# Optimization experiments

Measured on AMD Instinct MI355X. Metric: run time of the kernel, lower is better.

## Reference

```python
import jax, jax.numpy as jnp
import numpy as np

PI = 3.141592653
PC_RANGE = np.array([-140.8, -40.0, -3.0, 140.8, 40.0, 1.0], np.float32)
IOU_THR = 0.1


def limit_period(val, offset=0.5, period=2 * PI):
    return val - jnp.floor(val / period + offset) * period


def pairwise_iou3d(boxes):
    # Axis-aligned 3D IoU approximation of the external boxes_iou3d_gpu CUDA kernel
    # (kernel source not provided). boxes: [N,7] = x,y,z,h,w,l,yaw; extents x<-l, y<-w, z<-h.
    c = boxes[:, :3]
    d = boxes[:, jnp.array([5, 4, 3])]
    lo = c - d * 0.5
    hi = c + d * 0.5
    inter = jnp.clip(jnp.minimum(hi[:, None, :], hi[None, :, :]) - jnp.maximum(lo[:, None, :], lo[None, :, :]), 0.0)
    inter_v = inter.prod(-1)                       # [N,N]
    vol = d.prod(-1)                               # [N]
    return inter_v / jnp.maximum(vol[:, None] + vol[None, :] - inter_v, 1e-8)


def cluster_assign(iou):
    # Greedy sequential clustering: repeatedly take the first unassigned box and
    # assign every box with iou > 0.1 (including already-assigned ones -> overwrite)
    # to a new cluster id. Equivalent to the original while-loop since an index,
    # once nonzero, never returns to zero, so the "first zero" scans left-to-right.
    iou = jax.lax.stop_gradient(iou)
    n = iou.shape[0]

    def body(i, carry):
        idx, cid = carry
        is_new = idx[i] == 0
        idx = jnp.where(is_new & (iou[i] > IOU_THR), cid, idx)
        return idx, cid + jnp.where(is_new, 1, 0).astype(jnp.int32)

    idx0 = jnp.zeros(n, jnp.int32)
    idx, cid = jax.lax.fori_loop(0, n, body, (idx0, jnp.int32(1)))
    return idx, cid


def cluster_fusion(boxes, scores, indices):
    n = boxes.shape[0]
    ids = jnp.arange(1, n + 1, dtype=jnp.int32)
    M = indices[None, :] == ids[:, None]            # [K,N] membership, K==N (padded)
    s_m = jnp.where(M, scores[None, :], 0.0)        # masked scores
    s_sum = s_m.sum(1)
    s_norm = s_m / jnp.maximum(s_sum, 1e-12)[:, None]
    dirs = boxes[:, 6]
    ref_idx = jnp.argmax(jnp.where(M, scores[None, :], -jnp.inf), axis=1)
    ref_dir = dirs[ref_idx]                         # yaw of max-score box per cluster
    diff = jnp.abs(dirs[None, :] - ref_dir[:, None])
    diff = jnp.where(diff > PI, 2 * PI - diff, diff)
    gt = diff > PI / 2
    score_gt = (s_m * gt).sum(1)
    score_le = s_sum - score_gt
    flip = jnp.where((score_gt <= score_le)[:, None], gt, ~gt)
    dirs_adj = limit_period(dirs[None, :] + PI * flip)
    theta = jnp.arctan2((jnp.sin(dirs_adj) * s_norm).sum(1), (jnp.cos(dirs_adj) * s_norm).sum(1))
    center_dim = s_norm @ boxes[:, :6]              # [K,6] score-weighted fusion
    boxes_fused = jnp.concatenate([center_dim, theta[:, None]], axis=1)
    # score fusion: sum_i s_sorted[i] ** (i+1), clipped to 1 (zeros from padding contribute 0)
    s_sorted = jnp.sort(s_m, axis=1)[:, ::-1]
    powers = jnp.arange(1, n + 1, dtype=jnp.float32)
    s_fused = jnp.minimum((s_sorted ** powers[None, :]).sum(1), 1.0)
    member = M.any(1)
    return boxes_fused, s_fused, member


def boxes_to_corners_3d(boxes):
    # order 'hwl': dims = h,w,l; l along x, w along y, h along z; rotate about z by yaw
    x, y, z = boxes[:, 0], boxes[:, 1], boxes[:, 2]
    h, w, l = boxes[:, 3], boxes[:, 4], boxes[:, 5]
    yaw = boxes[:, 6]
    xs = jnp.array([1, 1, -1, -1, 1, 1, -1, -1], jnp.float32) * 0.5
    ys = jnp.array([-1, 1, 1, -1, -1, 1, 1, -1], jnp.float32) * 0.5
    zs = jnp.array([-1, -1, -1, -1, 1, 1, 1, 1], jnp.float32) * 0.5
    cx = l[:, None] * xs
    cy = w[:, None] * ys
    cz = h[:, None] * zs
    c_, s_ = jnp.cos(yaw)[:, None], jnp.sin(yaw)[:, None]
    rx = cx * c_ - cy * s_
    ry = cx * s_ + cy * c_
    return jnp.stack([rx + x[:, None], ry + y[:, None], cz + z[:, None]], axis=-1)  # [N,8,3]


def setup_inputs() -> dict:
    key = jax.random.key(0)
    k1, k2, k3, k4, k5, k6 = jax.random.split(key, 6)
    C, M = 512, 8                # 512 objects seen by 8 agents -> 4096 detections
    N = C * M
    cx = jax.random.uniform(k1, (C,), minval=-120.0, maxval=120.0)
    cy = jax.random.uniform(k2, (C,), minval=-35.0, maxval=35.0)
    centers = jnp.stack([cx, cy, jnp.zeros(C)], -1)                     # [C,3]
    pos = (centers[:, None, :] + jax.random.normal(k3, (C, M, 3)) * 0.3).reshape(N, 3)
    dims = jnp.array([[1.56, 1.84, 4.2]]) + jax.random.normal(k4, (N, 3)) * 0.05  # h,w,l
    base_yaw = jax.random.uniform(k5, (C, 1), minval=-PI, maxval=PI)
    yaw = (base_yaw + jax.random.normal(k6, (C, M)) * 0.1).reshape(N, 1)
    boxes = jnp.concatenate([pos, dims, yaw], axis=1).astype(jnp.float32)
    scores = jax.random.uniform(jax.random.fold_in(key, 9), (N,), minval=0.05, maxval=0.95).astype(jnp.float32)
    return {"boxes": boxes, "scores": scores}


def reference(boxes, scores):
    boxes = boxes.at[:, 6].set(limit_period(boxes[:, 6]))
    iou = pairwise_iou3d(boxes)
    indices, _ = cluster_assign(iou)
    boxes_f, scores_f, member = cluster_fusion(boxes, scores, indices)
    corners = boxes_to_corners_3d(boxes_f)
    in_range = ((corners[..., 0] > PC_RANGE[0]) & (corners[..., 0] < PC_RANGE[3]) &
                (corners[..., 1] > PC_RANGE[1]) & (corners[..., 1] < PC_RANGE[4])).all(1)
    valid = member & in_range
    newid = jnp.cumsum(valid.astype(jnp.int32))     # remap surviving cluster ids to 1..K'
    safe = jnp.maximum(indices - 1, 0)
    new_indices = jnp.where((indices > 0) & valid[safe], newid[safe], 0)
    boxes_out = jnp.where(valid[:, None], boxes_f, 0.0)
    scores_out = jnp.where(valid, scores_f, 0.0)
    return boxes_out, scores_out, valid, new_indices
```

## Files before the change

kernel.cpp:

```cpp
#include <hip/hip_runtime.h>
#include <math.h>

#define PI_F      3.141592653f
#define TWO_PI_F  6.283185306f
#define HALF_PI_F 1.5707963265f
#define IOU_THR_F 0.1f

typedef unsigned long long u64;

__device__ __forceinline__ float limit_period_f(float v) {
    return v - floorf(v / TWO_PI_F + 0.5f) * TWO_PI_F;
}

__global__ void adj_kernel(const float* __restrict__ boxes,
                           u64* __restrict__ adjC,
                           unsigned char* __restrict__ occByte,
                           int n, int words) {
    __shared__ float jS[7][64];
    int w = blockIdx.x;
    int tid = threadIdx.x;
    int lane = tid & 63, wv = tid >> 6;
    if (tid < 64) {
        int j = (w << 6) + tid;
        if (j < n) {
            float b0 = boxes[j*7+0], b1 = boxes[j*7+1], b2 = boxes[j*7+2];
            float b3 = boxes[j*7+3], b4 = boxes[j*7+4], b5 = boxes[j*7+5];
            jS[0][tid] = b0 - b5*0.5f;  jS[3][tid] = b0 + b5*0.5f;
            jS[1][tid] = b1 - b4*0.5f;  jS[4][tid] = b1 + b4*0.5f;
            jS[2][tid] = b2 - b3*0.5f;  jS[5][tid] = b2 + b3*0.5f;
            jS[6][tid] = (b5*b4)*b3;
        }
    }
    __syncthreads();
    int i = blockIdx.y * 256 + tid;
    u64 word = 0ull;
    if (i < n) {
        float b0 = boxes[i*7+0], b1 = boxes[i*7+1], b2 = boxes[i*7+2];
        float b3 = boxes[i*7+3], b4 = boxes[i*7+4], b5 = boxes[i*7+5];
        float lix = b0 - b5*0.5f, hix = b0 + b5*0.5f;
        float liy = b1 - b4*0.5f, hiy = b1 + b4*0.5f;
        float liz = b2 - b3*0.5f, hiz = b2 + b3*0.5f;
        float vi  = (b5*b4)*b3;
        int jmax = n - (w << 6); if (jmax > 64) jmax = 64;
        for (int jj = 0; jj < jmax; ++jj) {
            float ix = fminf(hix, jS[3][jj]) - fmaxf(lix, jS[0][jj]); ix = fmaxf(ix, 0.0f);
            float iy = fminf(hiy, jS[4][jj]) - fmaxf(liy, jS[1][jj]); iy = fmaxf(iy, 0.0f);
            float iz = fminf(hiz, jS[5][jj]) - fmaxf(liz, jS[2][jj]); iz = fmaxf(iz, 0.0f);
            float inter = (ix*iy)*iz;
            float u = fmaxf(vi + jS[6][jj] - inter, 1e-8f);
            bool pred = (inter / u) > IOU_THR_F;
            word |= ((u64)(pred ? 1 : 0)) << jj;
        }
        adjC[(size_t)w * n + i] = word;
    }
    u64 bal = __ballot((i < n) && word != 0ull);
    int rb = blockIdx.y * 4 + wv;
    if (lane == 0 && rb < 64)
        occByte[rb * 64 + w] = bal ? (unsigned char)1 : (unsigned char)0;
}

__global__ __launch_bounds__(1024) void mis_node_kernel(
        const u64* __restrict__ adjC,
        const unsigned char* __restrict__ occByte,
        int* __restrict__ indices,
        int* __restrict__ seedList,
        int* __restrict__ nclust,
        int n, int words) {
    __shared__ u64 S_l[64], R_l[64], occL[64];
    __shared__ int unresolved;
    __shared__ int wsS[64];
    int tid = threadIdx.x;
    int lane = tid & 63, wv = tid >> 6;

    for (int rb = wv; rb < 64; rb += 16) {
        unsigned char b = occByte[rb * 64 + lane];
        u64 m = __ballot(b != 0);
        if (lane == 0) occL[rb] = m;
    }
    if (tid < 64) {
        int base = tid << 6;
        int vb = n - base;
        u64 valid = (vb >= 64) ? ~0ull : ((vb <= 0) ? 0ull : ((1ull << vb) - 1ull));
        S_l[tid] = 0ull;
        R_l[tid] = ~valid;
    }
    __syncthreads();

    u64 nzm[4];
    int eA[4], eB[4], eC[4];
    u64 rA[4], rB[4], rC[4];
    u64 restM[4];
    #pragma unroll
    for (int k = 0; k < 4; ++k) {
        int i = (k << 10) + tid;
        u64 nz = 0ull, rest = 0ull;
        int cnt = 0;
        eA[k] = -1; eB[k] = -1; eC[k] = -1;
        rA[k] = 0ull; rB[k] = 0ull; rC[k] = 0ull;
        if (i < n) {
            int w_i = i >> 6, b_i = i & 63;
            u64 oc = occL[w_i];
            while (oc) {
                int e = (int)__ffsll(oc) - 1; oc &= oc - 1;
                if (e >= words) break;
                u64 row = adjC[(size_t)e * n + i];
                if (row) {
                    nz |= 1ull << e;
                    if (e <= w_i) {
                        u64 em = (e < w_i) ? ~0ull : (b_i ? ((1ull << b_i) - 1ull) : 0ull);
                        u64 re = row & em;
                        if (re) {
                            if      (cnt == 0) { eA[k] = e; rA[k] = re; }
                            else if (cnt == 1) { eB[k] = e; rB[k] = re; }
                            else if (cnt == 2) { eC[k] = e; rC[k] = re; }
                            else rest |= 1ull << e;
                            ++cnt;
                        }
                    }
                }
            }
        }
        nzm[k] = nz;
        restM[k] = rest;
    }

    unsigned done = 0;
    #pragma unroll
    for (int k = 0; k < 4; ++k)
        if (((k << 10) + tid) >= n) done |= 1u << k;

    for (;;) {
        if (tid == 0) unresolved = 0;
        unsigned pendSeed = 0, pendRes = 0;
        #pragma unroll
        for (int k = 0; k < 4; ++k) {
            if (done & (1u << k)) continue;
            int i = (k << 10) + tid;
            int w_i = i >> 6, b_i = i & 63;
            u64 sA = 0ull, uA = 0ull;
            if (eA[k] >= 0) { sA |= rA[k] & S_l[eA[k]]; uA |= rA[k] & ~R_l[eA[k]]; }
            if (eB[k] >= 0) { sA |= rB[k] & S_l[eB[k]]; uA |= rB[k] & ~R_l[eB[k]]; }
            if (eC[k] >= 0) { sA |= rC[k] & S_l[eC[k]]; uA |= rC[k] & ~R_l[eC[k]]; }
            u64 rm = restM[k];
            while (rm) {
                int e = (int)__ffsll(rm) - 1; rm &= rm - 1;
                u64 row = adjC[(size_t)e * n + i];
                u64 em = (e < w_i) ? ~0ull : (b_i ? ((1ull << b_i) - 1ull) : 0ull);
                sA |= row & S_l[e] & em;
                uA |= row & ~R_l[e] & em;
            }
            if (sA) pendRes |= 1u << k;
            else if (!uA) { pendSeed |= 1u << k; pendRes |= 1u << k; }
        }
        __syncthreads();
        #pragma unroll
        for (int k = 0; k < 4; ++k) {
            u64 bS = __ballot((pendSeed >> k) & 1u);
            u64 bR = __ballot((pendRes  >> k) & 1u);
            int w_i = ((k << 10) + tid) >> 6;
            if (lane == 0 && w_i < 64) {
                if (bS) atomicOr(&S_l[w_i], bS);
                if (bR) atomicOr(&R_l[w_i], bR);
            }
        }
        done |= pendRes;
        if ((done & 0xFu) != 0xFu) unresolved = 1;
        __syncthreads();
        if (unresolved == 0) break;
    }

    if (tid < 64) {
        int pc = (int)__popcll(S_l[tid]);
        int x = pc;
        for (int o = 1; o < 64; o <<= 1) {
            int y = __shfl_up(x, o);
            if (tid >= o) x += y;
        }
        wsS[tid] = x - pc;
        if (tid == 63) *nclust = x;
    }
    __syncthreads();
    #pragma unroll
    for (int k = 0; k < 4; ++k) {
        int i = (k << 10) + tid;
        if (i >= n) continue;
        int best = -1;
        u64 m = nzm[k];
        while (m) {
            int e = (int)__ffsll(m) - 1; m &= m - 1;
            u64 s = adjC[(size_t)e * n + i] & S_l[e];
            if (s) best = (e << 6) + 63 - (int)__clzll(s);
        }
        int idx = 0;
        if (best >= 0) {
            int w2 = best >> 6, b = best & 63;
            u64 incl = (b >= 63) ? ~0ull : ((2ull << b) - 1ull);
            idx = wsS[w2] + (int)__popcll(S_l[w2] & incl);
        }
        indices[i] = idx;
        int wj = i >> 6, bj = i & 63;
        if ((S_l[wj] >> bj) & 1ull) {
            int rank = wsS[wj] + (int)__popcll(S_l[wj] & (bj ? ((1ull << bj) - 1ull) : 0ull)) + 1;
            seedList[rank - 1] = i;
        }
    }
}

__global__ void fusion_kernel(const float* __restrict__ boxes,
                              const float* __restrict__ scores,
                              const int* __restrict__ indices,
                              const int* __restrict__ seedListG,
                              const int* __restrict__ nclust,
                              const u64* __restrict__ adjC,
                              float* __restrict__ fused,
                              float* __restrict__ sfused,
                              int* __restrict__ validArr, int n, int words) {
    int lane = threadIdx.x;
    int nc = *nclust;
    __shared__ unsigned short js[256];
    __shared__ float ms[256];
    __shared__ float ds[256];
    __shared__ float bx[6][256];
    __shared__ float sv[256], cv[256], pw[256];
    __shared__ float refdirS, denomS;
    __shared__ int   flipS, mS;
    for (int i = blockIdx.x; i < n; i += gridDim.x) {
        int cid = i + 1;
        if (cid > nc) {
            if (lane < 7) fused[i*7+lane] = 0.0f;
            if (lane == 0) { sfused[i] = 0.0f; validArr[i] = 0; }
            continue;
        }
        int s = seedListG[i];
        u64 bits = (lane < words) ? adjC[(size_t)lane * n + s] : 0ull;
        u64 keep = 0ull;
        u64 t = bits;
        while (t) {
            int b = (int)__ffsll(t) - 1;
            t &= t - 1;
            int node = (lane << 6) + b;
            if (indices[node] == cid) keep |= (1ull << b);
        }
        int cnt = __popcll(keep);
        int x = cnt;
        for (int o = 1; o < 64; o <<= 1) {
            int y = __shfl_up(x, o);
            if (lane >= o) x += y;
        }
        int excl = x - cnt;
        int m = __shfl(x, 63);
        int pos = excl;
        t = keep;
        while (t) {
            int b = (int)__ffsll(t) - 1;
            t &= t - 1;
            js[pos++] = (unsigned short)((lane << 6) + b);
        }
        __syncthreads();
        for (int k = lane; k < m; k += 64) {
            int j = js[k];
            ms[k] = scores[j];
            ds[k] = limit_period_f(boxes[j*7+6]);
            bx[0][k] = boxes[j*7+0];
            bx[1][k] = boxes[j*7+1];
            bx[2][k] = boxes[j*7+2];
            bx[3][k] = boxes[j*7+3];
            bx[4][k] = boxes[j*7+4];
            bx[5][k] = boxes[j*7+5];
        }
        __syncthreads();
        if (m == 0) {
            if (lane == 0) {
                for (int k = 0; k < 7; ++k) fused[i*7+k] = 0.0f;
                sfused[i] = 0.0f; validArr[i] = 0;
            }
            __syncthreads();
            continue;
        }
        if (lane == 0) {
            float ssum = 0.0f, smax = -1e30f; int kref = 0;
            for (int k = 0; k < m; ++k) {
                float sc = ms[k];
                ssum += sc;
                if (sc > smax) { smax = sc; kref = k; }
            }
            float refdir = ds[kref];
            float denom = fmaxf(ssum, 1e-12f);
            float sgt = 0.0f;
            for (int k = 0; k < m; ++k) {
                float d = fabsf(ds[k] - refdir);
                if (d > PI_F) d = TWO_PI_F - d;
                if (d > HALF_PI_F) sgt += ms[k];
            }
            float sle = ssum - sgt;
            refdirS = refdir; denomS = denom;
            flipS = (sgt <= sle) ? 1 : 0;
        }
        __syncthreads();
        {
            float refdir = refdirS, denom = denomS;
            bool flipGt = flipS != 0;
            for (int k = lane; k < m; k += 64) {
                float dj = ds[k];
                float d = fabsf(dj - refdir);
                if (d > PI_F) d = TWO_PI_F - d;
                bool gt = d > HALF_PI_F;
                bool flip = flipGt ? gt : !gt;
                float adj_d = limit_period_f(dj + (flip ? PI_F : 0.0f));
                float wgt = ms[k] / denom;
                sv[k] = sinf(adj_d) * wgt;
                cv[k] = cosf(adj_d) * wgt;
            }
        }
        __syncthreads();
        if (lane == 0) {
            float denom = denomS;
            float cd0=0,cd1=0,cd2=0,cd3=0,cd4=0,cd5=0;
            for (int k = 0; k < m; ++k) {
                float wgt = ms[k] / denom;
                cd0 += wgt * bx[0][k];
                cd1 += wgt * bx[1][k];
                cd2 += wgt * bx[2][k];
                cd3 += wgt * bx[3][k];
                cd4 += wgt * bx[4][k];
                cd5 += wgt * bx[5][k];
            }
            float ssin = 0.0f, scos = 0.0f;
            for (int k = 0; k < m; ++k) { ssin += sv[k]; scos += cv[k]; }
            float theta = atan2f(ssin, scos);
            for (int k = 1; k < m; ++k) {
                float key = ms[k]; int p = k - 1;
                while (p >= 0 && ms[p] < key) { ms[p+1] = ms[p]; --p; }
                ms[p+1] = key;
            }
            bx[0][255] = cd0; bx[1][255] = cd1; bx[2][255] = cd2;
            bx[3][255] = cd3; bx[4][255] = cd4; bx[5][255] = cd5;
            sv[255] = theta;
            mS = m;
        }
        __syncthreads();
        for (int k = lane; k < m; k += 64)
            pw[k] = powf(ms[k], (float)(k+1));
        __syncthreads();
        if (lane == 0) {
            float cd0 = bx[0][255], cd1 = bx[1][255], cd2 = bx[2][255];
            float cd3 = bx[3][255], cd4 = bx[4][255], cd5 = bx[5][255];
            float theta = sv[255];
            float sf = 0.0f;
            for (int k = 0; k < m; ++k) sf += pw[k];
            sf = fminf(sf, 1.0f);
            float c_ = cosf(theta), s_ = sinf(theta);
            float wdim = cd4, ldim = cd5;
            const float xs[4]  = {0.5f, 0.5f, -0.5f, -0.5f};
            const float ys_[4] = {-0.5f, 0.5f, 0.5f, -0.5f};
            bool inr = true;
            for (int c = 0; c < 4; ++c) {
                float cx = ldim * xs[c], cy = wdim * ys_[c];
                float rx = cx*c_ - cy*s_ + cd0;
                float ry = cx*s_ + cy*c_ + cd1;
                inr = inr && (rx > -140.8f) && (rx < 140.8f) && (ry > -40.0f) && (ry < 40.0f);
            }
            fused[i*7+0]=cd0; fused[i*7+1]=cd1; fused[i*7+2]=cd2;
            fused[i*7+3]=cd3; fused[i*7+4]=cd4; fused[i*7+5]=cd5;
            fused[i*7+6]=theta;
            sfused[i] = sf;
            validArr[i] = inr ? 1 : 0;
        }
        __syncthreads();
    }
}

__global__ void finalize_kernel(const float* __restrict__ fused,
                                const float* __restrict__ sfused,
                                const int* __restrict__ validArr,
                                const int* __restrict__ indices,
                                float* __restrict__ out, int n) {
    __shared__ int newidS[4096];
    __shared__ unsigned char validS[4096];
    __shared__ int scanBuf[1024];
    int tid = threadIdx.x;
    int per = (n + 1023) >> 10;
    int base = tid * per;
    int v[8];
    int sum = 0;
    for (int k = 0; k < per && k < 8; ++k) {
        int j = base + k;
        int vv = (j < n) ? validArr[j] : 0;
        v[k] = vv; sum += vv;
    }
    scanBuf[tid] = sum;
    __syncthreads();
    for (int o = 1; o < 1024; o <<= 1) {
        int val = scanBuf[tid];
        int add = (tid >= o) ? scanBuf[tid - o] : 0;
        __syncthreads();
        scanBuf[tid] = val + add;
        __syncthreads();
    }
    int run = scanBuf[tid] - sum;
    for (int k = 0; k < per && k < 8; ++k) {
        int j = base + k;
        if (j < n) { run += v[k]; newidS[j] = run; validS[j] = (unsigned char)v[k]; }
    }
    __syncthreads();
    float* boxesO  = out;
    float* scoresO = out + (size_t)7*n;
    float* validO  = out + (size_t)8*n;
    float* idxO    = out + (size_t)9*n;
    for (int j = tid; j < n; j += 1024) {
        int vv = validS[j];
        #pragma unroll
        for (int k = 0; k < 7; ++k)
            boxesO[j*7+k] = vv ? fused[j*7+k] : 0.0f;
        scoresO[j] = vv ? sfused[j] : 0.0f;
        validO[j]  = vv ? 1.0f : 0.0f;
        int ind = indices[j];
        int safe = ind - 1; if (safe < 0) safe = 0;
        bool nv = (ind > 0) && (validS[safe] != 0);
        idxO[j] = nv ? (float)newidS[safe] : 0.0f;
    }
}

extern "C" void kernel_launch(void* const* d_in, const int* in_sizes, int n_in,
                              void* d_out, int out_size, void* d_ws, size_t ws_size,
                              hipStream_t stream) {
    const float* boxes  = (const float*)d_in[0];
    const float* scores = (const float*)d_in[1];
    int n = in_sizes[0] / 7;
    int words = (n + 63) >> 6;

    char* ws = (char*)d_ws;
    size_t off = 0;
    u64* adjC = (u64*)(ws + off);
    off += (size_t)n * words * sizeof(u64);
    unsigned char* occByte = (unsigned char*)(ws + off); off += 64 * 64;
    int* seedList = (int*)(ws + off); off += (size_t)n * sizeof(int);
    int* indices  = (int*)(ws + off); off += (size_t)n * sizeof(int);
    float* fused  = (float*)(ws + off); off += (size_t)n * 7 * sizeof(float);
    float* sfused = (float*)(ws + off); off += (size_t)n * sizeof(float);
    int* validArr = (int*)(ws + off); off += (size_t)n * sizeof(int);
    int* nclust   = (int*)(ws + off); off += sizeof(int);

    dim3 adjGrid(words, (n + 255) / 256);
    adj_kernel<<<adjGrid, 256, 0, stream>>>(boxes, adjC, occByte, n, words);
    mis_node_kernel<<<1, 1024, 0, stream>>>(adjC, occByte, indices, seedList,
                                            nclust, n, words);
    fusion_kernel<<<512, 64, 0, stream>>>(boxes, scores, indices, seedList, nclust,
                                          adjC, fused, sfused, validArr, n, words);
    finalize_kernel<<<1, 1024, 0, stream>>>(fused, sfused, validArr, indices,
                                            (float*)d_out, n);
}
```

Before: 92.92 us.

## Split single-block MIS kernel into parallel prep, round, and indices kernels

The single-block MIS kernel is split into three launches. A 64-block prep kernel gathers each node's nonzero adjacency words (up to four cached rows plus an overflow mask). A single-block round kernel runs the iterative seed resolution from those compact arrays. A multi-block indices kernel computes cluster indices and the seed list, scanning from the highest word down so it can exit early. The aim is to move the serial gather and final assignment work off the lone 1024-thread block onto many blocks, at the cost of two extra launches and extra global-memory round trips.

Measured after the change: 82.27 us. -11.5%, faster.

```diff
diff --git a/kernel.cpp b/kernel.cpp
--- a/kernel.cpp
+++ b/kernel.cpp
@@ -59,24 +59,56 @@
         occByte[rb * 64 + w] = bal ? (unsigned char)1 : (unsigned char)0;
 }
 
-__global__ __launch_bounds__(1024) void mis_node_kernel(
+__global__ __launch_bounds__(64) void prep_kernel(
         const u64* __restrict__ adjC,
         const unsigned char* __restrict__ occByte,
-        int* __restrict__ indices,
-        int* __restrict__ seedList,
-        int* __restrict__ nclust,
-        int n, int words) {
-    __shared__ u64 S_l[64], R_l[64], occL[64];
+        u64* __restrict__ cRow, unsigned* __restrict__ idPack,
+        u64* __restrict__ restM, int n, int words) {
+    int rb = blockIdx.x;
+    int lane = threadIdx.x;
+    int i = (rb << 6) + lane;
+    unsigned char ob = occByte[rb * 64 + lane];
+    u64 occR = __ballot(ob != 0);
+    unsigned pack = 0xFFFFFFFFu;
+    u64 rest = 0ull;
+    u64 r0 = 0ull, r1 = 0ull, r2 = 0ull, r3 = 0ull;
+    int cnt = 0;
+    if (i < n) {
+        u64 oc = occR;
+        while (oc) {
+            int e = (int)__ffsll(oc) - 1; oc &= oc - 1;
+            if (e >= words) break;
+            u64 row = adjC[(size_t)e * n + i];
+            if (row) {
+                if      (cnt == 0) { r0 = row; pack = (pack & 0xFFFFFF00u) | (unsigned)e; }
+                else if (cnt == 1) { r1 = row; pack = (pack & 0xFFFF00FFu) | ((unsigned)e << 8); }
+                else if (cnt == 2) { r2 = row; pack = (pack & 0xFF00FFFFu) | ((unsigned)e << 16); }
+                else if (cnt == 3) { r3 = row; pack = (pack & 0x00FFFFFFu) | ((unsigned)e << 24); }
+                else rest |= 1ull << e;
+                ++cnt;
+            }
+        }
+    }
+    if (i < n) {
+        cRow[(size_t)0 * n + i] = r0;
+        cRow[(size_t)1 * n + i] = r1;
+        cRow[(size_t)2 * n + i] = r2;
+        cRow[(size_t)3 * n + i] = r3;
+        idPack[i] = pack;
+        restM[i]  = rest;
+    }
+}
+
+__global__ __launch_bounds__(1024) void mis_round_kernel(
+        const u64* __restrict__ adjC,
+        const u64* __restrict__ cRow, const unsigned* __restrict__ idPack,
+        const u64* __restrict__ restM,
+        u64* __restrict__ SG, int n, int words) {
+    __shared__ u64 S_l[64], R_l[64];
     __shared__ int unresolved;
-    __shared__ int wsS[64];
     int tid = threadIdx.x;
-    int lane = tid & 63, wv = tid >> 6;
-
-    for (int rb = wv; rb < 64; rb += 16) {
-        unsigned char b = occByte[rb * 64 + lane];
-        u64 m = __ballot(b != 0);
-        if (lane == 0) occL[rb] = m;
-    }
+    int lane = tid & 63;
+
     if (tid < 64) {
         int base = tid << 6;
         int vb = n - base;
@@ -86,42 +118,27 @@
     }
     __syncthreads();
 
-    u64 nzm[4];
-    int eA[4], eB[4], eC[4];
-    u64 rA[4], rB[4], rC[4];
-    u64 restM[4];
+    int id0[4], id1[4], id2[4], id3[4];
+    u64 r0[4], r1[4], r2[4], r3[4], rstR[4];
     #pragma unroll
     for (int k = 0; k < 4; ++k) {
         int i = (k << 10) + tid;
-        u64 nz = 0ull, rest = 0ull;
-        int cnt = 0;
-        eA[k] = -1; eB[k] = -1; eC[k] = -1;
-        rA[k] = 0ull; rB[k] = 0ull; rC[k] = 0ull;
+        id0[k] = id1[k] = id2[k] = id3[k] = 0xFF;
+        r0[k] = r1[k] = r2[k] = r3[k] = 0ull; rstR[k] = 0ull;
         if (i < n) {
-            int w_i = i >> 6, b_i = i & 63;
-            u64 oc = occL[w_i];
-            while (oc) {
-                int e = (int)__ffsll(oc) - 1; oc &= oc - 1;
-                if (e >= words) break;
-                u64 row = adjC[(size_t)e * n + i];
-                if (row) {
-                    nz |= 1ull << e;
-                    if (e <= w_i) {
-                        u64 em = (e < w_i) ? ~0ull : (b_i ? ((1ull << b_i) - 1ull) : 0ull);
-                        u64 re = row & em;
-                        if (re) {
-                            if      (cnt == 0) { eA[k] = e; rA[k] = re; }
-                            else if (cnt == 1) { eB[k] = e; rB[k] = re; }
-                            else if (cnt == 2) { eC[k] = e; rC[k] = re; }
-                            else rest |= 1ull << e;
-                            ++cnt;
-                        }
-                    }
-                }
-            }
-        }
-        nzm[k] = nz;
-        restM[k] = rest;
+            unsigned p = idPack[i];
+            id0[k] = (int)(p & 0xFFu);
+            id1[k] = (int)((p >> 8) & 0xFFu);
+            id2[k] = (int)((p >> 16) & 0xFFu);
+            id3[k] = (int)((p >> 24) & 0xFFu);
+            r0[k] = cRow[(size_t)0 * n + i];
+            r1[k] = cRow[(size_t)1 * n + i];
+            r2[k] = cRow[(size_t)2 * n + i];
+            r3[k] = cRow[(size_t)3 * n + i];
+            int w_i = i >> 6;
+            u64 inclm = (w_i >= 63) ? ~0ull : ((2ull << w_i) - 1ull);
+            rstR[k] = restM[i] & inclm;
+        }
     }
 
     unsigned done = 0;
@@ -137,15 +154,20 @@
             if (done & (1u << k)) continue;
             int i = (k << 10) + tid;
             int w_i = i >> 6, b_i = i & 63;
+            u64 lowm = b_i ? ((1ull << b_i) - 1ull) : 0ull;
             u64 sA = 0ull, uA = 0ull;
-            if (eA[k] >= 0) { sA |= rA[k] & S_l[eA[k]]; uA |= rA[k] & ~R_l[eA[k]]; }
-            if (eB[k] >= 0) { sA |= rB[k] & S_l[eB[k]]; uA |= rB[k] & ~R_l[eB[k]]; }
-            if (eC[k] >= 0) { sA |= rC[k] & S_l[eC[k]]; uA |= rC[k] & ~R_l[eC[k]]; }
-            u64 rm = restM[k];
+            #define RACC(IDV, RV) if (IDV != 0xFF && IDV <= w_i) { \
+                u64 em = (IDV < w_i) ? ~0ull : lowm; \
+                u64 mr = (RV) & em; \
+                sA |= mr & S_l[IDV]; uA |= mr & ~R_l[IDV]; }
+            RACC(id0[k], r0[k]) RACC(id1[k], r1[k])
+            RACC(id2[k], r2[k]) RACC(id3[k], r3[k])
+            #undef RACC
+            u64 rm = rstR[k];
             while (rm) {
                 int e = (int)__ffsll(rm) - 1; rm &= rm - 1;
                 u64 row = adjC[(size_t)e * n + i];
-                u64 em = (e < w_i) ? ~0ull : (b_i ? ((1ull << b_i) - 1ull) : 0ull);
+                u64 em = (e < w_i) ? ~0ull : lowm;
                 sA |= row & S_l[e] & em;
                 uA |= row & ~R_l[e] & em;
             }
@@ -168,41 +190,66 @@
         __syncthreads();
         if (unresolved == 0) break;
     }
-
-    if (tid < 64) {
-        int pc = (int)__popcll(S_l[tid]);
-        int x = pc;
-        for (int o = 1; o < 64; o <<= 1) {
-            int y = __shfl_up(x, o);
-            if (tid >= o) x += y;
-        }
-        wsS[tid] = x - pc;
-        if (tid == 63) *nclust = x;
-    }
+    if (tid < 64) SG[tid] = S_l[tid];
+}
+
+__global__ __launch_bounds__(64) void indices_kernel(
+        const u64* __restrict__ adjC,
+        const u64* __restrict__ SG,
+        const u64* __restrict__ cRow, const unsigned* __restrict__ idPack,
+        const u64* __restrict__ restM,
+        int* __restrict__ indices, int* __restrict__ seedList,
+        int* __restrict__ nclust, int n, int words) {
+    __shared__ u64 S_s[64];
+    __shared__ int ws_s[64];
+    int lane = threadIdx.x;
+    u64 s = (lane < words) ? SG[lane] : 0ull;
+    S_s[lane] = s;
+    int pc = (int)__popcll(s);
+    int x = pc;
+    for (int o = 1; o < 64; o <<= 1) {
+        int y = __shfl_up(x, o);
+        if (lane >= o) x += y;
+    }
+    ws_s[lane] = x - pc;
+    if (blockIdx.x == 0 && lane == 63) *nclust = x;
     __syncthreads();
-    #pragma unroll
-    for (int k = 0; k < 4; ++k) {
-        int i = (k << 10) + tid;
-        if (i >= n) continue;
-        int best = -1;
-        u64 m = nzm[k];
-        while (m) {
-            int e = (int)__ffsll(m) - 1; m &= m - 1;
-            u64 s = adjC[(size_t)e * n + i] & S_l[e];
-            if (s) best = (e << 6) + 63 - (int)__clzll(s);
-        }
-        int idx = 0;
-        if (best >= 0) {
-            int w2 = best >> 6, b = best & 63;
-            u64 incl = (b >= 63) ? ~0ull : ((2ull << b) - 1ull);
-            idx = wsS[w2] + (int)__popcll(S_l[w2] & incl);
-        }
-        indices[i] = idx;
-        int wj = i >> 6, bj = i & 63;
-        if ((S_l[wj] >> bj) & 1ull) {
-            int rank = wsS[wj] + (int)__popcll(S_l[wj] & (bj ? ((1ull << bj) - 1ull) : 0ull)) + 1;
-            seedList[rank - 1] = i;
-        }
+    int i = blockIdx.x * 64 + lane;
+    if (i >= n) return;
+    unsigned p = idPack[i];
+    u64 c0 = cRow[(size_t)0 * n + i];
+    u64 c1 = cRow[(size_t)1 * n + i];
+    u64 c2 = cRow[(size_t)2 * n + i];
+    u64 c3 = cRow[(size_t)3 * n + i];
+    int best = -1;
+    u64 rm = restM[i];
+    while (rm) {
+        int e = 63 - (int)__clzll(rm); rm &= ~(1ull << e);
+        u64 s2 = adjC[(size_t)e * n + i] & S_s[e];
+        if (s2) { best = (e << 6) + 63 - (int)__clzll(s2); break; }
+    }
+    if (best < 0) {
+        #define ITRY(IDV, CV) if (best < 0 && (IDV) != 0xFFu) { \
+            int e = (int)(IDV); \
+            u64 s2 = (CV) & S_s[e]; \
+            if (s2) best = (e << 6) + 63 - (int)__clzll(s2); }
+        ITRY((p >> 24) & 0xFFu, c3)
+        ITRY((p >> 16) & 0xFFu, c2)
+        ITRY((p >> 8) & 0xFFu, c1)
+        ITRY(p & 0xFFu, c0)
+        #undef ITRY
+    }
+    int idx = 0;
+    if (best >= 0) {
+        int w2 = best >> 6, b = best & 63;
+        u64 incl = (b >= 63) ? ~0ull : ((2ull << b) - 1ull);
+        idx = ws_s[w2] + (int)__popcll(S_s[w2] & incl);
+    }
+    indices[i] = idx;
+    int wj = i >> 6, bj = i & 63;
+    if ((S_s[wj] >> bj) & 1ull) {
+        int rank = ws_s[wj] + (int)__popcll(S_s[wj] & (bj ? ((1ull << bj) - 1ull) : 0ull)) + 1;
+        seedList[rank - 1] = i;
     }
 }
 
@@ -434,6 +481,10 @@
     u64* adjC = (u64*)(ws + off);
     off += (size_t)n * words * sizeof(u64);
     unsigned char* occByte = (unsigned char*)(ws + off); off += 64 * 64;
+    u64* cRow   = (u64*)(ws + off); off += (size_t)4 * n * sizeof(u64);
+    unsigned* idPack = (unsigned*)(ws + off); off += (size_t)n * sizeof(unsigned);
+    u64* restM  = (u64*)(ws + off); off += (size_t)n * sizeof(u64);
+    u64* SG     = (u64*)(ws + off); off += 64 * sizeof(u64);
     int* seedList = (int*)(ws + off); off += (size_t)n * sizeof(int);
     int* indices  = (int*)(ws + off); off += (size_t)n * sizeof(int);
     float* fused  = (float*)(ws + off); off += (size_t)n * 7 * sizeof(float);
@@ -443,8 +494,10 @@
 
     dim3 adjGrid(words, (n + 255) / 256);
     adj_kernel<<<adjGrid, 256, 0, stream>>>(boxes, adjC, occByte, n, words);
-    mis_node_kernel<<<1, 1024, 0, stream>>>(adjC, occByte, indices, seedList,
-                                            nclust, n, words);
+    prep_kernel<<<64, 64, 0, stream>>>(adjC, occByte, cRow, idPack, restM, n, words);
+    mis_round_kernel<<<1, 1024, 0, stream>>>(adjC, cRow, idPack, restM, SG, n, words);
+    indices_kernel<<<(n + 63) / 64, 64, 0, stream>>>(adjC, SG, cRow, idPack, restM,
+                                                     indices, seedList, nclust, n, words);
     fusion_kernel<<<512, 64, 0, stream>>>(boxes, scores, indices, seedList, nclust,
                                           adjC, fused, sfused, validArr, n, words);
     finalize_kernel<<<1, 1024, 0, stream>>>(fused, sfused, validArr, indices,
```
